# Kernel tuning notes

Hardware: AMD Instinct MI355X
Metric: run time of the kernel (lower is better)

## Reference

```python
import jax, jax.numpy as jnp
import numpy as np
import math

B, L, D = 8, 2048, 256
NUM_TYPES = 1
T_MAX = 200.0
SIGMA = 1.0


def setup_inputs() -> dict:
    key = jax.random.key(0)
    ks = jax.random.split(key, 12)
    event_type = jnp.ones((B, L), dtype=jnp.int64 if jax.config.jax_enable_x64 else jnp.int32)
    t = jax.random.uniform(ks[0], (B, L), dtype=jnp.float32) * T_MAX
    event_time = jnp.sort(t, axis=-1)
    s = 1.0 / math.sqrt(D)
    emb_weight = jax.random.normal(ks[1], (NUM_TYPES + 1, D), jnp.float32)
    emb_weight = emb_weight.at[0].set(0.0)  # padding_idx=0
    gate_w = jax.random.normal(ks[2], (2, D), jnp.float32) * s
    gate_b = jnp.zeros((2,), jnp.float32)
    ker_w = jax.random.normal(ks[3], (1, D), jnp.float32) * s
    ker_b = jnp.zeros((1,), jnp.float32)
    ln_gamma = jnp.ones((D,), jnp.float32)
    ln_beta = jnp.zeros((D,), jnp.float32)
    gen_input_w = jax.random.normal(ks[4], (D, D), jnp.float32) * s
    gen_noise_w = jax.random.normal(ks[5], (D, D), jnp.float32) * s
    gen_out_w = jax.random.normal(ks[6], (1, D), jnp.float32) * s
    gen_out_b = jnp.zeros((1,), jnp.float32)
    noise = jax.random.uniform(ks[7], (B, L, D), jnp.float32)  # torch.rand noise in Generator
    return dict(event_type=event_type, event_time=event_time, emb_weight=emb_weight,
                gate_w=gate_w, gate_b=gate_b, ker_w=ker_w, ker_b=ker_b,
                ln_gamma=ln_gamma, ln_beta=ln_beta, gen_input_w=gen_input_w,
                gen_noise_w=gen_noise_w, gen_out_w=gen_out_w, gen_out_b=gen_out_b,
                noise=noise)


def _softplus_beta(x, beta):
    return jax.nn.softplus(beta * x) / beta


def reference(event_type, event_time, emb_weight, gate_w, gate_b, ker_w, ker_b,
              ln_gamma, ln_beta, gen_input_w, gen_noise_w, gen_out_w, gen_out_b, noise):
    d_model = emb_weight.shape[-1]
    # ---- temporal positional encoding (this is `embedding`) ----
    pos_vec = jnp.power(10000.0, 2.0 * jnp.arange(d_model, dtype=jnp.float32) / d_model)
    t = event_time[:, :, None] / pos_vec                      # [B,L,D]
    idx = jnp.arange(d_model)
    temp_enc = jnp.where(idx % 2 == 0, jnp.sin(t), jnp.cos(t))
    # ---- type embedding ----
    te = emb_weight[event_type] * math.sqrt(d_model)          # [B,L,D]
    # ---- pairwise |t_i - t_j| ; xt[b,i,j]=t_i, xt_bar[b,i,j]=t_j ----
    dt = jnp.abs(event_time[:, :, None] - event_time[:, None, :])  # [B,L,L]
    # ---- squared exponential kernel: params depend only on row i (xd[b,i,j]=te[b,i]) ----
    ls = _softplus_beta(te @ ker_w.T + ker_b, 0.2)[..., 0]    # [B,L]
    scores_k = (SIGMA ** 2) * jnp.exp(-(dt ** 2) / (ls[:, :, None] ** 2))
    # ---- sigmoid gate ----
    p = jax.nn.sigmoid(te @ gate_w.T + gate_b)                # [B,L,2]
    l = p[..., 0][:, :, None]
    s = p[..., 1][:, :, None]
    gate = 1.0 + 0.5 * jnp.tanh((dt / T_MAX - l) / s)
    scores = scores_k * gate                                  # [B,L,L]
    # ---- causal mask: strictly-upper-triangle -> -1e10, then softmax ----
    causal = jnp.tril(jnp.ones((event_time.shape[1], event_time.shape[1]), jnp.bool_))
    scores = jnp.where(causal[None], scores, -1e10)
    attn = jax.nn.softmax(scores, axis=-1)
    # ---- hidden = attn @ temp_enc, layernorm ----
    hidden = jnp.einsum('bij,bjd->bid', attn, temp_enc)
    mu = hidden.mean(-1, keepdims=True)
    var = hidden.var(-1, keepdims=True)
    hidden = (hidden - mu) / jnp.sqrt(var + 1e-6) * ln_gamma + ln_beta
    # ---- Generator (dropout in eval = identity) ----
    h = jax.nn.relu(noise @ gen_noise_w.T + hidden @ gen_input_w.T)
    out = jax.nn.softplus(h @ gen_out_w.T + gen_out_b)[..., 0]  # [B,L]
    return out
```

## Files before the change

kernel.cpp:

```cpp
#include <hip/hip_runtime.h>
#include <hip/hip_bf16.h>

#define BD 8
#define LD 2048
#define DD 256

typedef unsigned short ushort_t;
typedef __attribute__((ext_vector_type(8))) short short8;
typedef __attribute__((ext_vector_type(4))) float floatx4;

__device__ __forceinline__ ushort_t f2bfu(float x) {
  __hip_bfloat16 h = __float2bfloat16(x);
  return *reinterpret_cast<ushort_t*>(&h);
}

__device__ __forceinline__ void dma16(const ushort_t* g, ushort_t* l) {
  __builtin_amdgcn_global_load_lds(
      (const __attribute__((address_space(1))) unsigned int*)g,
      (__attribute__((address_space(3))) unsigned int*)l,
      16, 0, 0);
}

__device__ __forceinline__ float sin_acc(float a) {
  float k = rintf(a * 0.15915494f);
  float r = __builtin_fmaf(-k, 6.2831855f, a);
  r = __builtin_fmaf(-k, -1.7484555e-7f, r);
  return __sinf(r);
}
__device__ __forceinline__ float cos_acc(float a) {
  float k = rintf(a * 0.15915494f);
  float r = __builtin_fmaf(-k, 6.2831855f, a);
  r = __builtin_fmaf(-k, -1.7484555e-7f, r);
  return __cosf(r);
}

__global__ __launch_bounds__(256) void k_prep(
    const int* __restrict__ etype, const float* __restrict__ etime,
    const float* __restrict__ embw, const float* __restrict__ gatew,
    const float* __restrict__ gateb, const float* __restrict__ kerw,
    const float* __restrict__ kerb, const float* __restrict__ noise,
    const float* __restrict__ wn, const float* __restrict__ wi,
    ushort_t* __restrict__ enc_bf, ushort_t* __restrict__ noise_bf,
    ushort_t* __restrict__ wcat, float* __restrict__ ptable)
{
  const int bk = blockIdx.x;
  const int tid = threadIdx.x;
  if (bk < 4224) {
    int idx = bk * 256 + tid;
    if (idx < 1048576) {
      float4 f = ((const float4*)noise)[idx];
      ushort4 u;
      u.x = f2bfu(f.x); u.y = f2bfu(f.y); u.z = f2bfu(f.z); u.w = f2bfu(f.w);
      *(ushort4*)(noise_bf + (size_t)idx * 4) = u;
    } else {
      int p = idx - 1048576;
      int c = p >> 7;
      int k = (p & 127) * 4;
      const float* src = (k < 256) ? (wn + c * 256 + k) : (wi + c * 256 + (k - 256));
      float4 f = *(const float4*)src;
      ushort4 u;
      u.x = f2bfu(f.x); u.y = f2bfu(f.y); u.z = f2bfu(f.z); u.w = f2bfu(f.w);
      *(ushort4*)(wcat + (size_t)c * 512 + k) = u;
    }
  } else if (bk < 4736) {
    int ebk = bk - 4224;
    __shared__ float ts[32];
    if (tid < 32) ts[tid] = etime[(ebk >> 6) * LD + (ebk & 63) * 32 + tid];
    __syncthreads();
    uint4* dst = (uint4*)(enc_bf + (size_t)ebk * 8192);
    const int jb = (tid & 3) * 8;
    #pragma unroll
    for (int jblk = 0; jblk < 4; ++jblk) {
      int d = jblk * 64 + (tid >> 2);
      float freq = __expf(-0.07195578416f * (float)d);
      unsigned int pk[4];
      #pragma unroll
      for (int p = 0; p < 4; ++p) {
        float a0 = ts[jb + 2 * p] * freq;
        float a1 = ts[jb + 2 * p + 1] * freq;
        float v0 = (d & 1) ? cos_acc(a0) : sin_acc(a0);
        float v1 = (d & 1) ? cos_acc(a1) : sin_acc(a1);
        pk[p] = (unsigned int)f2bfu(v0) | ((unsigned int)f2bfu(v1) << 16);
      }
      dst[jblk * 256 + tid] = make_uint4(pk[0], pk[1], pk[2], pk[3]);
    }
  } else {
    __shared__ float red[4][3];
    int lane = tid & 63, wvi = tid >> 6;
    for (int ty = 0; ty < 2; ++ty) {
      float te = embw[ty * DD + tid] * 16.0f;
      float p1 = te * kerw[tid];
      float p2 = te * gatew[tid];
      float p3 = te * gatew[DD + tid];
      #pragma unroll
      for (int off = 32; off > 0; off >>= 1) {
        p1 += __shfl_xor(p1, off);
        p2 += __shfl_xor(p2, off);
        p3 += __shfl_xor(p3, off);
      }
      if (lane == 0) { red[wvi][0] = p1; red[wvi][1] = p2; red[wvi][2] = p3; }
      __syncthreads();
      if (tid == 0) {
        float s1 = red[0][0] + red[1][0] + red[2][0] + red[3][0] + kerb[0];
        float s2 = red[0][1] + red[1][1] + red[2][1] + red[3][1] + gateb[0];
        float s3 = red[0][2] + red[1][2] + red[2][2] + red[3][2] + gateb[1];
        float z = 0.2f * s1;
        float sp = (z > 15.0f) ? z : log1pf(__expf(z));
        float ls = 5.0f * sp;
        ptable[ty * 4 + 0] = 1.0f / (ls * ls);
        ptable[ty * 4 + 1] = 1.0f / (1.0f + __expf(-s2));
        float s = 1.0f / (1.0f + __expf(-s3));
        ptable[ty * 4 + 2] = 1.0f / s;
      }
      __syncthreads();
    }
  }
}

__global__ __launch_bounds__(256, 4) void k_attn(
    const ushort_t* __restrict__ enc_bf, const float* __restrict__ etime,
    const int* __restrict__ etype, const float* __restrict__ ptable,
    const float* __restrict__ gamma, const float* __restrict__ beta,
    ushort_t* __restrict__ hidden_bf)
{
  __shared__ __align__(16) ushort_t stage[2][8192];
  const int tid = threadIdx.x;
  const int lane = tid & 63, wv = tid >> 6;
  const int bk = blockIdx.x;
  const int b = bk & 7;
  const int rb = 63 - (bk >> 3);
  const int base = b * LD;
  const int m = lane & 15, kg = lane >> 4;
  const int tile = 2 * rb + (wv >> 1);
  const int p = wv & 1;
  const int i = tile * 16 + m;
  const float ti = etime[base + i];
  const int ty = etype[base + i];
  const float il = ptable[ty * 4 + 0];
  const float ll = ptable[ty * 4 + 1];
  const float is2 = 2.0f * ptable[ty * 4 + 2];
  floatx4 acc[16];
  #pragma unroll
  for (int nt = 0; nt < 16; ++nt) acc[nt] = (floatx4){0.f, 0.f, 0.f, 0.f};
  const int nch = rb + 1;
  const ushort_t* __restrict__ encC = enc_bf + (size_t)(b * 64) * 8192;
  const int fr0 = wv * 4;
  const int boff = m * 32 + kg * 8;
  {
    const ushort_t* g = encC + fr0 * 512 + lane * 8;
    #pragma unroll
    for (int q = 0; q < 4; ++q) dma16(g + q * 512, &stage[0][(fr0 + q) * 512]);
  }
  float tj[8];
  if (p == 0) {
    float4 a = *(const float4*)(etime + base + kg * 8);
    float4 c = *(const float4*)(etime + base + kg * 8 + 4);
    tj[0] = a.x; tj[1] = a.y; tj[2] = a.z; tj[3] = a.w;
    tj[4] = c.x; tj[5] = c.y; tj[6] = c.z; tj[7] = c.w;
  }
  for (int ch = 0; ch < nch; ++ch) {
    const int cur = ch & 1;
    const bool mine = ((ch & 1) == p);
    short8 af;
    if (mine) {
      const int j0 = ch * 32 + kg * 8;
      #pragma unroll
      for (int v = 0; v < 8; ++v) {
        float dt = ti - tj[v];
        float sk = __expf(-dt * dt * il);
        float rg = __builtin_amdgcn_rcpf(__expf((dt * 0.005f - ll) * is2) + 1.0f);
        float w = __expf(sk * (1.5f - rg));
        w = (j0 + v <= i) ? w : 0.0f;
        af[v] = (short)f2bfu(w);
      }
    }
    __syncthreads();
    if (ch + 1 < nch) {
      const ushort_t* g = encC + (size_t)(ch + 1) * 8192 + fr0 * 512 + lane * 8;
      #pragma unroll
      for (int q = 0; q < 4; ++q) dma16(g + q * 512, &stage[cur ^ 1][(fr0 + q) * 512]);
      if (((ch + 1) & 1) == p) {
        const int j0n = (ch + 1) * 32 + kg * 8;
        float4 a = *(const float4*)(etime + base + j0n);
        float4 c = *(const float4*)(etime + base + j0n + 4);
        tj[0] = a.x; tj[1] = a.y; tj[2] = a.z; tj[3] = a.w;
        tj[4] = c.x; tj[5] = c.y; tj[6] = c.z; tj[7] = c.w;
      }
    }
    if (mine) {
      #pragma unroll
      for (int nt = 0; nt < 16; ++nt) {
        short8 bf = *(const short8*)(&stage[cur][nt * 512 + boff]);
        acc[nt] = __builtin_amdgcn_mfma_f32_16x16x32_bf16(af, bf, acc[nt], 0, 0, 0);
      }
    }
  }
  __syncthreads();
  floatx4* reg0 = (floatx4*)&stage[0][0];
  floatx4* reg1 = (floatx4*)&stage[1][0];
  if (wv == 1) {
    #pragma unroll
    for (int nt = 0; nt < 16; ++nt) reg0[nt * 64 + lane] = acc[nt];
  } else if (wv == 3) {
    #pragma unroll
    for (int nt = 0; nt < 16; ++nt) reg1[nt * 64 + lane] = acc[nt];
  }
  __syncthreads();
  if ((wv & 1) == 0) {
    floatx4* reg = (wv == 0) ? reg0 : reg1;
    #pragma unroll
    for (int nt = 0; nt < 16; ++nt) acc[nt] += reg[nt * 64 + lane];
    float gl[16], cl[16];
    #pragma unroll
    for (int nt = 0; nt < 16; ++nt) { gl[nt] = gamma[nt * 16 + m]; cl[nt] = beta[nt * 16 + m]; }
    const int q = lane >> 4;
    #pragma unroll
    for (int r = 0; r < 4; ++r) {
      float h[16];
      float sm = 0.0f, sq = 0.0f;
      #pragma unroll
      for (int nt = 0; nt < 16; ++nt) {
        h[nt] = acc[nt][r];
        sm += h[nt]; sq += h[nt] * h[nt];
      }
      #pragma unroll
      for (int off = 1; off < 16; off <<= 1) {
        sm += __shfl_xor(sm, off);
        sq += __shfl_xor(sq, off);
      }
      float mean = sm * (1.0f / 256.0f);
      float var = sq * (1.0f / 256.0f) - mean * mean;
      float rstd = rsqrtf(var + 1e-6f);
      const int row = q * 4 + r;
      ushort_t* dst = hidden_bf + ((size_t)(base + tile * 16 + row)) * DD + m;
      #pragma unroll
      for (int nt = 0; nt < 16; ++nt)
        dst[nt * 16] = f2bfu((h[nt] - mean) * rstd * gl[nt] + cl[nt]);
    }
  }
}

__global__ __launch_bounds__(256) void k_gen(
    const ushort_t* __restrict__ noise_bf, const ushort_t* __restrict__ hidden_bf,
    const ushort_t* __restrict__ wcat, const float* __restrict__ wout,
    const float* __restrict__ bout, float* __restrict__ out)
{
  __shared__ float pbuf[4][2][16];
  const int tid = threadIdx.x;
  const int lane = tid & 63, wv = tid >> 6;
  const int m = lane & 15, kg = lane >> 4;
  const int r0 = blockIdx.x * 32 + m;
  const ushort_t* __restrict__ an0 = noise_bf + (size_t)r0 * DD;
  const ushort_t* __restrict__ an1 = noise_bf + (size_t)(r0 + 16) * DD;
  const ushort_t* __restrict__ ah0 = hidden_bf + (size_t)r0 * DD;
  const ushort_t* __restrict__ ah1 = hidden_bf + (size_t)(r0 + 16) * DD;
  floatx4 acc[2][4];
  #pragma unroll
  for (int t = 0; t < 2; ++t)
    #pragma unroll
    for (int n = 0; n < 4; ++n) acc[t][n] = (floatx4){0.f, 0.f, 0.f, 0.f};
  const ushort_t* __restrict__ bbase = wcat + ((size_t)(wv * 4) * 16 + m) * 512 + kg * 8;
  #pragma unroll
  for (int ks = 0; ks < 16; ++ks) {
    const int koff = (ks & 7) * 32 + kg * 8;
    short8 a0 = *(const short8*)(((ks < 8) ? an0 : ah0) + koff);
    short8 a1 = *(const short8*)(((ks < 8) ? an1 : ah1) + koff);
    const ushort_t* bp = bbase + ks * 32;
    #pragma unroll
    for (int n = 0; n < 4; ++n) {
      short8 bf = *(const short8*)(bp + (size_t)n * 8192);
      acc[0][n] = __builtin_amdgcn_mfma_f32_16x16x32_bf16(a0, bf, acc[0][n], 0, 0, 0);
      acc[1][n] = __builtin_amdgcn_mfma_f32_16x16x32_bf16(a1, bf, acc[1][n], 0, 0, 0);
    }
  }
  float wo_l[4];
  #pragma unroll
  for (int n = 0; n < 4; ++n) wo_l[n] = wout[(wv * 4 + n) * 16 + m];
  #pragma unroll
  for (int t = 0; t < 2; ++t) {
    #pragma unroll
    for (int r4 = 0; r4 < 4; ++r4) {
      float p = 0.0f;
      #pragma unroll
      for (int n = 0; n < 4; ++n) p += fmaxf(acc[t][n][r4], 0.0f) * wo_l[n];
      #pragma unroll
      for (int off = 1; off < 16; off <<= 1) p += __shfl_xor(p, off);
      if (m == 0) pbuf[wv][t][kg * 4 + r4] = p;
    }
  }
  __syncthreads();
  if (tid < 32) {
    int t = tid >> 4, rr = tid & 15;
    float x = pbuf[0][t][rr] + pbuf[1][t][rr] + pbuf[2][t][rr] + pbuf[3][t][rr] + bout[0];
    float sp = (x > 15.0f) ? x : log1pf(__expf(x));
    out[blockIdx.x * 32 + t * 16 + rr] = sp;
  }
}

extern "C" void kernel_launch(void* const* d_in, const int* in_sizes, int n_in,
                              void* d_out, int out_size, void* d_ws, size_t ws_size,
                              hipStream_t stream) {
  const int*   etype = (const int*)d_in[0];
  const float* etime = (const float*)d_in[1];
  const float* embw  = (const float*)d_in[2];
  const float* gatew = (const float*)d_in[3];
  const float* gateb = (const float*)d_in[4];
  const float* kerw  = (const float*)d_in[5];
  const float* kerb  = (const float*)d_in[6];
  const float* gamma = (const float*)d_in[7];
  const float* beta  = (const float*)d_in[8];
  const float* wi    = (const float*)d_in[9];
  const float* wn    = (const float*)d_in[10];
  const float* wo    = (const float*)d_in[11];
  const float* bo    = (const float*)d_in[12];
  const float* noise = (const float*)d_in[13];
  float* out = (float*)d_out;

  char* w8 = (char*)d_ws;
  float* ptable       = (float*)(w8);
  ushort_t* enc_bf    = (ushort_t*)(w8 + 262144);
  ushort_t* hidden_bf = (ushort_t*)(w8 + 262144 + 8388608);
  ushort_t* noise_bf  = (ushort_t*)(w8 + 262144 + 2 * 8388608);
  ushort_t* wcat      = (ushort_t*)(w8 + 262144 + 3 * 8388608);

  k_prep<<<4737, 256, 0, stream>>>(etype, etime, embw, gatew, gateb, kerw, kerb,
                                   noise, wn, wi, enc_bf, noise_bf, wcat, ptable);
  k_attn<<<512, 256, 0, stream>>>(enc_bf, etime, etype, ptable,
                                  gamma, beta, hidden_bf);
  k_gen<<<512, 256, 0, stream>>>(noise_bf, hidden_bf, wcat, wo, bo, out);
}
```

Measured before the change: 183.1 us.

## Split attention into 128-thread blocks with per-wave independent DMA pipelines

Each attention block now handles a single 16-row tile with two waves instead of two tiles with four. Each wave streams its own alternating chunks into private LDS buffers, using manual waitcnt-based double buffering in place of block-wide __syncthreads per chunk. This removes barrier stalls and lets each wave overlap DMA with MFMA work. The generator weight matrix is also re-laid out into tiles so each B-fragment load is contiguous. Hand-coded waitcnt immediates risk hazards if the vmcnt encoding or the count of outstanding loads is wrong.

```diff
diff --git a/kernel.cpp b/kernel.cpp
--- a/kernel.cpp
+++ b/kernel.cpp
@@ -20,6 +20,11 @@
       (__attribute__((address_space(3))) unsigned int*)l,
       16, 0, 0);
 }
+
+#define WAIT_VM0  0x0F70
+#define WAIT_VM8  0x0F78
+#define WAIT_VM10 0x0F7A
+#define WAIT_LGKM 0xC07F
 
 __device__ __forceinline__ float sin_acc(float a) {
   float k = rintf(a * 0.15915494f);
@@ -60,7 +65,8 @@
       float4 f = *(const float4*)src;
       ushort4 u;
       u.x = f2bfu(f.x); u.y = f2bfu(f.y); u.z = f2bfu(f.z); u.w = f2bfu(f.w);
-      *(ushort4*)(wcat + (size_t)c * 512 + k) = u;
+      *(ushort4*)(wcat + (((size_t)(c >> 4) * 16 + (k >> 5)) * 512)
+                       + (c & 15) * 32 + (k & 31)) = u;
     }
   } else if (bk < 4736) {
     int ebk = bk - 4224;
@@ -117,23 +123,21 @@
   }
 }
 
-__global__ __launch_bounds__(256, 4) void k_attn(
+__global__ __launch_bounds__(128) void k_attn(
     const ushort_t* __restrict__ enc_bf, const float* __restrict__ etime,
     const int* __restrict__ etype, const float* __restrict__ ptable,
     const float* __restrict__ gamma, const float* __restrict__ beta,
     ushort_t* __restrict__ hidden_bf)
 {
-  __shared__ __align__(16) ushort_t stage[2][8192];
+  __shared__ __align__(16) ushort_t stage[2][2][4096];
   const int tid = threadIdx.x;
   const int lane = tid & 63, wv = tid >> 6;
   const int bk = blockIdx.x;
   const int b = bk & 7;
-  const int rb = 63 - (bk >> 3);
+  const int tl = 127 - (bk >> 3);
   const int base = b * LD;
   const int m = lane & 15, kg = lane >> 4;
-  const int tile = 2 * rb + (wv >> 1);
-  const int p = wv & 1;
-  const int i = tile * 16 + m;
+  const int i = tl * 16 + m;
   const float ti = etime[base + i];
   const int ty = etype[base + i];
   const float il = ptable[ty * 4 + 0];
@@ -142,28 +146,28 @@
   floatx4 acc[16];
   #pragma unroll
   for (int nt = 0; nt < 16; ++nt) acc[nt] = (floatx4){0.f, 0.f, 0.f, 0.f};
-  const int nch = rb + 1;
+  const int nch = tl / 2 + 1;
+  const int myn = (nch > wv) ? ((nch - wv + 1) >> 1) : 0;
   const ushort_t* __restrict__ encC = enc_bf + (size_t)(b * 64) * 8192;
-  const int fr0 = wv * 4;
   const int boff = m * 32 + kg * 8;
-  {
-    const ushort_t* g = encC + fr0 * 512 + lane * 8;
-    #pragma unroll
-    for (int q = 0; q < 4; ++q) dma16(g + q * 512, &stage[0][(fr0 + q) * 512]);
-  }
-  float tj[8];
-  if (p == 0) {
-    float4 a = *(const float4*)(etime + base + kg * 8);
-    float4 c = *(const float4*)(etime + base + kg * 8 + 4);
-    tj[0] = a.x; tj[1] = a.y; tj[2] = a.z; tj[3] = a.w;
-    tj[4] = c.x; tj[5] = c.y; tj[6] = c.z; tj[7] = c.w;
-  }
-  for (int ch = 0; ch < nch; ++ch) {
-    const int cur = ch & 1;
-    const bool mine = ((ch & 1) == p);
+  ushort_t* bufA = &stage[wv][0][0];
+  ushort_t* bufB = &stage[wv][1][0];
+
+  if (myn > 0) {
+    const int c0 = wv;
+    float4 ta = *(const float4*)(etime + base + c0 * 32 + kg * 8);
+    float4 tc = *(const float4*)(etime + base + c0 * 32 + kg * 8 + 4);
+    {
+      const ushort_t* g = encC + (size_t)c0 * 8192 + lane * 8;
+      #pragma unroll
+      for (int q = 0; q < 8; ++q) dma16(g + q * 512, bufA + q * 512);
+      #pragma unroll
+      for (int q = 0; q < 8; ++q) dma16(g + (q + 8) * 512, bufB + q * 512);
+    }
+    float tj[8] = {ta.x, ta.y, ta.z, ta.w, tc.x, tc.y, tc.z, tc.w};
     short8 af;
-    if (mine) {
-      const int j0 = ch * 32 + kg * 8;
+    {
+      const int j0 = c0 * 32 + kg * 8;
       #pragma unroll
       for (int v = 0; v < 8; ++v) {
         float dt = ti - tj[v];
@@ -174,40 +178,59 @@
         af[v] = (short)f2bfu(w);
       }
     }
-    __syncthreads();
-    if (ch + 1 < nch) {
-      const ushort_t* g = encC + (size_t)(ch + 1) * 8192 + fr0 * 512 + lane * 8;
-      #pragma unroll
-      for (int q = 0; q < 4; ++q) dma16(g + q * 512, &stage[cur ^ 1][(fr0 + q) * 512]);
-      if (((ch + 1) & 1) == p) {
-        const int j0n = (ch + 1) * 32 + kg * 8;
-        float4 a = *(const float4*)(etime + base + j0n);
-        float4 c = *(const float4*)(etime + base + j0n + 4);
-        tj[0] = a.x; tj[1] = a.y; tj[2] = a.z; tj[3] = a.w;
-        tj[4] = c.x; tj[5] = c.y; tj[6] = c.z; tj[7] = c.w;
-      }
-    }
-    if (mine) {
-      #pragma unroll
-      for (int nt = 0; nt < 16; ++nt) {
-        short8 bf = *(const short8*)(&stage[cur][nt * 512 + boff]);
-        acc[nt] = __builtin_amdgcn_mfma_f32_16x16x32_bf16(af, bf, acc[nt], 0, 0, 0);
+    for (int idx = 0; idx < myn; ++idx) {
+      const int ch = wv + 2 * idx;
+      const bool more = (idx + 1 < myn);
+      const int cn = more ? (ch + 2) : wv;
+      __builtin_amdgcn_s_waitcnt(WAIT_VM8);
+      #pragma unroll
+      for (int q = 0; q < 8; ++q) {
+        short8 bf = *(const short8*)(bufA + q * 512 + boff);
+        acc[q] = __builtin_amdgcn_mfma_f32_16x16x32_bf16(af, bf, acc[q], 0, 0, 0);
+      }
+      float4 na = *(const float4*)(etime + base + cn * 32 + kg * 8);
+      float4 nc = *(const float4*)(etime + base + cn * 32 + kg * 8 + 4);
+      __builtin_amdgcn_s_waitcnt(WAIT_LGKM);
+      {
+        const ushort_t* g = encC + (size_t)cn * 8192 + lane * 8;
+        #pragma unroll
+        for (int q = 0; q < 8; ++q) dma16(g + q * 512, bufA + q * 512);
+      }
+      __builtin_amdgcn_s_waitcnt(WAIT_VM10);
+      #pragma unroll
+      for (int q = 0; q < 8; ++q) {
+        short8 bf = *(const short8*)(bufB + q * 512 + boff);
+        acc[8 + q] = __builtin_amdgcn_mfma_f32_16x16x32_bf16(af, bf, acc[8 + q], 0, 0, 0);
+      }
+      __builtin_amdgcn_s_waitcnt(WAIT_LGKM);
+      {
+        const ushort_t* g = encC + (size_t)cn * 8192 + lane * 8;
+        #pragma unroll
+        for (int q = 0; q < 8; ++q) dma16(g + (q + 8) * 512, bufB + q * 512);
+      }
+      if (more) {
+        float ntj[8] = {na.x, na.y, na.z, na.w, nc.x, nc.y, nc.z, nc.w};
+        const int j0 = cn * 32 + kg * 8;
+        #pragma unroll
+        for (int v = 0; v < 8; ++v) {
+          float dt = ti - ntj[v];
+          float sk = __expf(-dt * dt * il);
+          float rg = __builtin_amdgcn_rcpf(__expf((dt * 0.005f - ll) * is2) + 1.0f);
+          float w = __expf(sk * (1.5f - rg));
+          w = (j0 + v <= i) ? w : 0.0f;
+          af[v] = (short)f2bfu(w);
+        }
       }
     }
   }
   __syncthreads();
-  floatx4* reg0 = (floatx4*)&stage[0][0];
-  floatx4* reg1 = (floatx4*)&stage[1][0];
+  floatx4* reg = (floatx4*)&stage[0][0][0];
   if (wv == 1) {
     #pragma unroll
-    for (int nt = 0; nt < 16; ++nt) reg0[nt * 64 + lane] = acc[nt];
-  } else if (wv == 3) {
-    #pragma unroll
-    for (int nt = 0; nt < 16; ++nt) reg1[nt * 64 + lane] = acc[nt];
+    for (int nt = 0; nt < 16; ++nt) reg[nt * 64 + lane] = acc[nt];
   }
   __syncthreads();
-  if ((wv & 1) == 0) {
-    floatx4* reg = (wv == 0) ? reg0 : reg1;
+  if (wv == 0) {
     #pragma unroll
     for (int nt = 0; nt < 16; ++nt) acc[nt] += reg[nt * 64 + lane];
     float gl[16], cl[16];
@@ -232,7 +255,7 @@
       float var = sq * (1.0f / 256.0f) - mean * mean;
       float rstd = rsqrtf(var + 1e-6f);
       const int row = q * 4 + r;
-      ushort_t* dst = hidden_bf + ((size_t)(base + tile * 16 + row)) * DD + m;
+      ushort_t* dst = hidden_bf + ((size_t)(base + tl * 16 + row)) * DD + m;
       #pragma unroll
       for (int nt = 0; nt < 16; ++nt)
         dst[nt * 16] = f2bfu((h[nt] - mean) * rstd * gl[nt] + cl[nt]);
@@ -259,16 +282,16 @@
   for (int t = 0; t < 2; ++t)
     #pragma unroll
     for (int n = 0; n < 4; ++n) acc[t][n] = (floatx4){0.f, 0.f, 0.f, 0.f};
-  const ushort_t* __restrict__ bbase = wcat + ((size_t)(wv * 4) * 16 + m) * 512 + kg * 8;
+  const int slot = m * 32 + kg * 8;
   #pragma unroll
   for (int ks = 0; ks < 16; ++ks) {
     const int koff = (ks & 7) * 32 + kg * 8;
     short8 a0 = *(const short8*)(((ks < 8) ? an0 : ah0) + koff);
     short8 a1 = *(const short8*)(((ks < 8) ? an1 : ah1) + koff);
-    const ushort_t* bp = bbase + ks * 32;
     #pragma unroll
     for (int n = 0; n < 4; ++n) {
-      short8 bf = *(const short8*)(bp + (size_t)n * 8192);
+      const ushort_t* bp = wcat + ((size_t)(wv * 4 + n) * 16 + ks) * 512 + slot;
+      short8 bf = *(const short8*)bp;
       acc[0][n] = __builtin_amdgcn_mfma_f32_16x16x32_bf16(a0, bf, acc[0][n], 0, 0, 0);
       acc[1][n] = __builtin_amdgcn_mfma_f32_16x16x32_bf16(a1, bf, acc[1][n], 0, 0, 0);
     }
@@ -325,7 +348,7 @@
 
   k_prep<<<4737, 256, 0, stream>>>(etype, etime, embw, gatew, gateb, kerw, kerb,
                                    noise, wn, wi, enc_bf, noise_bf, wcat, ptable);
-  k_attn<<<512, 256, 0, stream>>>(enc_bf, etime, etype, ptable,
-                                  gamma, beta, hidden_bf);
+  k_attn<<<1024, 128, 0, stream>>>(enc_bf, etime, etype, ptable,
+                                   gamma, beta, hidden_bf);
   k_gen<<<512, 256, 0, stream>>>(noise_bf, hidden_bf, wcat, wo, bo, out);
 }
```

Measured after the change: 163.5 us. 10.7% less time.
